# Optimization experiments

Measured on AMD Instinct MI355X. Metric: run time of the kernel, lower is better.

## Reference

```python
import jax, jax.numpy as jnp
import numpy as np

B, M, K, KNN = 2, 256, 64, 16
CXYZ, CFEAT = 3, 61
CIN = CXYZ + CFEAT  # 64
MLPS = [64, 128]
SUMM = sum(MLPS)    # 192
CALIB = 64
EXP = [256, 512]
OUT = 256
EPS = 1e-5


def bn(x, g, b):
    # BatchNorm eval mode with running_mean=0, running_var=1 (channel axis 1)
    shape = (1, -1) + (1,) * (x.ndim - 2)
    return x * (g / jnp.sqrt(1.0 + EPS)).reshape(shape) + b.reshape(shape)


def knn(x, k):
    xx = jnp.sum(x * x, axis=1)                      # (B, N)
    inner = jnp.einsum('bcn,bcm->bnm', x, x)         # (B, N, N)
    pd = 2.0 * inner - xx[:, :, None] - xx[:, None, :]
    return jax.lax.top_k(pd, k)[1]                   # (B, N, k)


def graph_feature(x, idx):
    # x: (B, C, N), idx: (B, N, k) -> (B, 2C, N, k)
    xt = jnp.transpose(x, (0, 2, 1))                 # (B, N, C)
    nb = jax.vmap(lambda a, i: a[i])(xt, idx)        # (B, N, k, C)
    ctr = xt[:, :, None, :]
    feat = jnp.concatenate([nb - ctr, jnp.broadcast_to(ctr, nb.shape)], axis=-1)
    return jnp.transpose(feat, (0, 3, 1, 2))


def forward(xyz, feats, e1_w, e1_g, e1_b, e2_w, e2_g, e2_b,
            cal1_w, cal1_g, cal1_b, cal2_w, cal2_bias,
            exp1_w, exp1_g, exp1_b, exp2_w, exp2_g, exp2_b,
            red_w, red_g, red_b, sc1_w, sc1_b, sc2_w, sc2_b,
            sc_n1_g, sc_n1_b, sc_n2_g, sc_n2_b):
    x3 = xyz.reshape(B * M, K, CXYZ).transpose(0, 2, 1)      # (BM, 3, K)
    f = feats.reshape(B * M, K, CFEAT).transpose(0, 2, 1)    # (BM, 61, K)
    idx = knn(x3, KNN)                                        # USE_FEATS_DIS=False: knn once on xyz
    x = jnp.concatenate([x3, f], axis=1)                      # (BM, 64, K)
    outs = []
    for W, g, b in ((e1_w, e1_g, e1_b), (e2_w, e2_g, e2_b)):
        gf = graph_feature(x, idx)                            # (BM, 2C, K, knn)
        y = jax.nn.relu(bn(jnp.einsum('oc,bcnk->bonk', W, gf), g, b))
        x = y.max(axis=-1)                                    # (BM, mlp_i, K)
        outs.append(x)
    x = jnp.concatenate(outs, axis=1)                         # (BM, 192, K)
    c = jax.nn.relu(bn(jnp.einsum('oc,bcn->bon', cal1_w, x), cal1_g, cal1_b))
    c = jnp.einsum('oc,bcn->bon', cal2_w, c) + cal2_bias[None, :, None]
    x = jax.nn.sigmoid(c) * x
    x = jax.nn.relu(bn(jnp.einsum('oc,bcn->bon', exp1_w, x), exp1_g, exp1_b))
    x = jax.nn.relu(bn(jnp.einsum('oc,bcn->bon', exp2_w, x), exp2_g, exp2_b))
    x = x.max(axis=-1).reshape(B, M, EXP[1]).transpose(0, 2, 1)  # (B, 512, M)
    x = jax.nn.relu(bn(jnp.einsum('oc,bcm->bom', red_w, x), red_g, red_b))
    x = bn(x + x, sc_n1_g, sc_n1_b)
    h = jax.nn.relu(jnp.einsum('oc,bcm->bom', sc1_w, x) + sc1_b[None, :, None])
    h = jnp.einsum('oc,bcm->bom', sc2_w, h) + sc2_b[None, :, None]
    x = bn(x + h, sc_n2_g, sc_n2_b)
    return x                                                  # (B, 256, M)


def setup_inputs() -> dict:
    key = jax.random.key(0)
    ks = jax.random.split(key, 16)
    w = lambda k, s: jax.random.normal(k, s, jnp.float32) * 0.05
    ones = lambda n: jnp.ones((n,), jnp.float32)
    zeros = lambda n: jnp.zeros((n,), jnp.float32)
    return {
        'xyz': jax.random.normal(ks[0], (B, M, K, CXYZ), jnp.float32),
        'feats': jax.random.normal(ks[1], (B, M, K, CFEAT), jnp.float32),
        'e1_w': w(ks[2], (MLPS[0], 2 * CIN)), 'e1_g': ones(MLPS[0]), 'e1_b': zeros(MLPS[0]),
        'e2_w': w(ks[3], (MLPS[1], 2 * MLPS[0])), 'e2_g': ones(MLPS[1]), 'e2_b': zeros(MLPS[1]),
        'cal1_w': w(ks[4], (CALIB, SUMM)), 'cal1_g': ones(CALIB), 'cal1_b': zeros(CALIB),
        'cal2_w': w(ks[5], (SUMM, CALIB)), 'cal2_bias': zeros(SUMM),
        'exp1_w': w(ks[6], (EXP[0], SUMM)), 'exp1_g': ones(EXP[0]), 'exp1_b': zeros(EXP[0]),
        'exp2_w': w(ks[7], (EXP[1], EXP[0])), 'exp2_g': ones(EXP[1]), 'exp2_b': zeros(EXP[1]),
        'red_w': w(ks[8], (OUT, EXP[1])), 'red_g': ones(OUT), 'red_b': zeros(OUT),
        'sc1_w': w(ks[9], (OUT, OUT)), 'sc1_b': zeros(OUT),
        'sc2_w': w(ks[10], (OUT, OUT)), 'sc2_b': zeros(OUT),
        'sc_n1_g': ones(OUT), 'sc_n1_b': zeros(OUT),
        'sc_n2_g': ones(OUT), 'sc_n2_b': zeros(OUT),
    }


def reference(xyz, feats, e1_w, e1_g, e1_b, e2_w, e2_g, e2_b,
              cal1_w, cal1_g, cal1_b, cal2_w, cal2_bias,
              exp1_w, exp1_g, exp1_b, exp2_w, exp2_g, exp2_b,
              red_w, red_g, red_b, sc1_w, sc1_b, sc2_w, sc2_b,
              sc_n1_g, sc_n1_b, sc_n2_g, sc_n2_b):
    return forward(xyz, feats, e1_w, e1_g, e1_b, e2_w, e2_g, e2_b,
                   cal1_w, cal1_g, cal1_b, cal2_w, cal2_bias,
                   exp1_w, exp1_g, exp1_b, exp2_w, exp2_g, exp2_b,
                   red_w, red_g, red_b, sc1_w, sc1_b, sc2_w, sc2_b,
                   sc_n1_g, sc_n1_b, sc_n2_g, sc_n2_b)
```

## Files before the change

kernel.cpp:

```cpp
#include <hip/hip_runtime.h>
#include <hip/hip_bf16.h>
#include <math.h>
#include <stddef.h>

#define DEV __device__ __forceinline__
__device__ const float BNS = 0.99999500003749968f;

typedef __bf16 bf16x8 __attribute__((ext_vector_type(8)));
typedef float  f32x4  __attribute__((ext_vector_type(4)));

DEV unsigned short f2bs(float v){
  union{ __hip_bfloat16 b; unsigned short u; } c; c.b=__float2bfloat16(v); return c.u;
}
DEV float bs2f(unsigned short u){
  union{ unsigned short u; __hip_bfloat16 b; } c; c.u=u; return __bfloat162float(c.b);
}


__global__ __launch_bounds__(256) void k_prep(const float* __restrict__ e1_w,
    const float* __restrict__ e2_w, const float* __restrict__ cal1_w,
    const float* __restrict__ cal2_w, const float* __restrict__ exp1_w,
    const float* __restrict__ exp2_w, unsigned short* __restrict__ Whi,
    unsigned short* __restrict__ Wlo){
  int bid = blockIdx.x;
  const float* src; unsigned short *hi,*lo; int mode, O=0, i0;
  if(bid<32)      { src=e1_w;  hi=Whi;       lo=Wlo;       mode=1; O= 64; i0=bid*256; }
  else if(bid<96) { src=e2_w;  hi=Whi+8192;  lo=Wlo+8192;  mode=1; O=128; i0=(bid-32)*256; }
  else if(bid<144){ src=cal1_w;hi=Whi+24576; lo=Wlo+24576; mode=0;        i0=(bid-96)*256; }
  else if(bid<192){ src=cal2_w;hi=Whi+36864; lo=Wlo+36864; mode=0;        i0=(bid-144)*256; }
  else if(bid<384){ src=exp1_w;hi=Whi+49152; lo=Wlo+49152; mode=0;        i0=(bid-192)*256; }
  else            { src=exp2_w;hi=Whi+98304; lo=Wlo+98304; mode=0;        i0=(bid-384)*256; }
  int i = i0 + threadIdx.x;
  float v;
  if(mode==0) v = src[i];
  else {
    int row=i>>6, c=i&63;
    v = (row<O) ? src[row*128+c] : (src[(row-O)*128+64+c]-src[(row-O)*128+c]);
  }
  unsigned short h=f2bs(v); hi[i]=h; lo[i]=f2bs(v-bs2f(h));
}

__global__ __launch_bounds__(256) void k_knn(const float* __restrict__ xyz,
    const float* __restrict__ feats, int* __restrict__ idxo,
    unsigned short* __restrict__ x0s){
  int bm = blockIdx.x;
  int tid = threadIdx.x, n = tid&63, s = tid>>6;
  __shared__ float sx0[64], sx1[64], sx2[64], sxx[64];
  __shared__ float pd[64][65];
  __shared__ float cv[64][4];
  __shared__ int   ci[64][4];
  __shared__ unsigned short sb[64*130];
  if(s==0){
    const float* xp = xyz + (size_t)(bm*64+n)*3;
    float px=xp[0], py=xp[1], pz=xp[2];
    sx0[n]=px; sx1[n]=py; sx2[n]=pz; sxx[n]=px*px+py*py+pz*pz;
  }
  __syncthreads();
  float px=sx0[n], py=sx1[n], pz=sx2[n], xxn=sxx[n];
  #pragma unroll
  for(int t=0;t<16;t++){
    int m = s*16+t;
    float inner = px*sx0[m]+py*sx1[m]+pz*sx2[m];
    pd[n][m] = 2.0f*inner - xxn - sxx[m];
  }
  __syncthreads();
  int* ip = idxo + bm*1024 + n*16;
  for(int j=0;j<16;j++){
    float best=-3.4e38f; int bi=s*16;
    #pragma unroll
    for(int t=0;t<16;t++){ int m=s*16+t; float v=pd[n][m]; if(v>best){best=v;bi=m;} }
    cv[n][s]=best; ci[n][s]=bi;
    __syncthreads();
    if(s==0){
      float bb=cv[n][0]; int bj=ci[n][0];
      #pragma unroll
      for(int q2=1;q2<4;q2++){ if(cv[n][q2]>bb){bb=cv[n][q2]; bj=ci[n][q2];} }
      ip[j]=bj; pd[n][bj]=-3.4e38f;
    }
    __syncthreads();
  }
  unsigned short* r = sb + n*130;
  if(s==0){
    unsigned short h;
    h=f2bs(px); r[0]=h; r[64]=f2bs(px-bs2f(h));
    h=f2bs(py); r[1]=h; r[65]=f2bs(py-bs2f(h));
    h=f2bs(pz); r[2]=h; r[66]=f2bs(pz-bs2f(h));
  }
  const float* fp = feats + (size_t)(bm*64+n)*61;
  #pragma unroll
  for(int t=0;t<16;t++){
    int cc = s*16+t;
    if(cc<61){
      float v=fp[cc]; unsigned short h=f2bs(v);
      r[3+cc]=h; r[64+3+cc]=f2bs(v-bs2f(h));
    }
  }
  __syncthreads();
  unsigned int* g32 = (unsigned int*)(x0s + (size_t)bm*8192);
  const unsigned int* s32 = (const unsigned int*)sb;
  #pragma unroll
  for(int t=0;t<16;t++){ int i=s*16+t; g32[i*64+n]=s32[i*65+n]; }
}

template<int O>
__global__ __launch_bounds__(256) void k_edge2(
    const unsigned short* __restrict__ Wh, const unsigned short* __restrict__ Wl,
    const unsigned short* __restrict__ X, int RS, int LO,
    const int* __restrict__ idxg, const float* __restrict__ gg,
    const float* __restrict__ bb, unsigned short* __restrict__ cat, int coloff){
  __shared__ float zs[64*65];
  __shared__ float ds[64*65];
  int bm = blockIdx.x;
  int tid = threadIdx.x, wid = tid>>6, lane = tid&63;
  int l15 = lane&15, q = lane>>4;
  const int* ip0 = idxg + bm*1024;
  size_t xrow = ((size_t)bm*64 + l15)*RS;
  for(int ch=0; ch<O/64; ch++){
    int rbase = ((wid<2)?0:O) + ch*64 + (wid&1)*32;
    f32x4 acc[2][4];
    #pragma unroll
    for(int a=0;a<2;a++)
      #pragma unroll
      for(int d=0;d<4;d++) acc[a][d]=(f32x4){0.f,0.f,0.f,0.f};
    #pragma unroll
    for(int kc=0;kc<2;kc++){
      int k0=kc*32;
      size_t a0=(size_t)(rbase+l15)*64 + k0 + q*8;
      size_t a1=(size_t)(rbase+16+l15)*64 + k0 + q*8;
      bf16x8 a0h=*(const bf16x8*)(Wh+a0), a0l=*(const bf16x8*)(Wl+a0);
      bf16x8 a1h=*(const bf16x8*)(Wh+a1), a1l=*(const bf16x8*)(Wl+a1);
      #pragma unroll
      for(int nt=0;nt<4;nt++){
        const unsigned short* xp = X + xrow + (size_t)nt*16*RS + k0 + q*8;
        bf16x8 bh=*(const bf16x8*)xp, bl=*(const bf16x8*)(xp+LO);
        acc[0][nt]=__builtin_amdgcn_mfma_f32_16x16x32_bf16(a0h,bh,acc[0][nt],0,0,0);
        acc[0][nt]=__builtin_amdgcn_mfma_f32_16x16x32_bf16(a0h,bl,acc[0][nt],0,0,0);
        acc[0][nt]=__builtin_amdgcn_mfma_f32_16x16x32_bf16(a0l,bh,acc[0][nt],0,0,0);
        acc[1][nt]=__builtin_amdgcn_mfma_f32_16x16x32_bf16(a1h,bh,acc[1][nt],0,0,0);
        acc[1][nt]=__builtin_amdgcn_mfma_f32_16x16x32_bf16(a1h,bl,acc[1][nt],0,0,0);
        acc[1][nt]=__builtin_amdgcn_mfma_f32_16x16x32_bf16(a1l,bh,acc[1][nt],0,0,0);
      }
    }
    __syncthreads();
    float* dst = (wid<2)? zs : ds;
    int ro = (wid&1)*32;
    #pragma unroll
    for(int mt=0;mt<2;mt++)
      #pragma unroll
      for(int nt=0;nt<4;nt++)
        #pragma unroll
        for(int rr=0;rr<4;rr++)
          dst[(ro+mt*16+q*4+rr)*65 + nt*16+l15] = acc[mt][nt][rr];
    __syncthreads();
    int o = ch*64 + lane;
    float s = gg[o]*BNS, bi = bb[o];
    #pragma unroll 4
    for(int j=0;j<16;j++){
      int n = wid*16 + j;
      const int* ip = ip0 + n*16;
      float mz = -3.4e38f;
      #pragma unroll
      for(int k=0;k<16;k++) mz = fmaxf(mz, zs[lane*65 + ip[k]]);
      float v = fmaxf(s*(mz + ds[lane*65 + n]) + bi, 0.f);
      unsigned short hv = f2bs(v);
      size_t cb = ((size_t)bm*64+n)*384 + coloff + o;
      cat[cb] = hv; cat[cb+192] = f2bs(v - bs2f(hv));
    }
    __syncthreads();
  }
}

template<int K, int BO, int EPI>
__global__ __launch_bounds__(256) void k_mm2(
    const unsigned short* __restrict__ Whi, const unsigned short* __restrict__ Wlo,
    const unsigned short* __restrict__ X, void* __restrict__ Og,
    const float* __restrict__ sg, const float* __restrict__ bg, int O){
  constexpr int WO = BO/4;
  constexpr int MT = WO/16;
  constexpr int WUNITS = BO*8;
  __shared__ __align__(16) unsigned short sW[BO*64];
  __shared__ __align__(16) unsigned short sX[128*64];
  int rt = blockIdx.x;
  int o0 = blockIdx.y*BO;
  int tid = threadIdx.x, wid = tid>>6, lane = tid&63;
  int l15 = lane&15, q = lane>>4;
  f32x4 acc[MT][8];
  #pragma unroll
  for(int a=0;a<MT;a++)
    #pragma unroll
    for(int d=0;d<8;d++) acc[a][d]=(f32x4){0.f,0.f,0.f,0.f};
  size_t xbase = (size_t)rt*128*2*K;
  for(int kc=0; kc<K/32; kc++){
    int k0 = kc*32;
    __syncthreads();
    #pragma unroll
    for(int i=0;i<WUNITS/256;i++){
      int U = tid + i*256;
      int r = U>>3, up = U&7, u = up ^ (r&7);
      const unsigned short* src = (u<4)
        ? (Whi + (size_t)(o0+r)*K + k0 + u*8)
        : (Wlo + (size_t)(o0+r)*K + k0 + (u-4)*8);
      *(uint4*)&sW[U*8] = *(const uint4*)src;
    }
    #pragma unroll
    for(int i=0;i<4;i++){
      int U = tid + i*256;
      int r = U>>3, up = U&7, u = up ^ (r&7);
      const unsigned short* src = X + xbase + (size_t)r*2*K
        + (u<4 ? (size_t)(k0 + u*8) : (size_t)(K + k0 + (u-4)*8));
      *(uint4*)&sX[U*8] = *(const uint4*)src;
    }
    __syncthreads();
    bf16x8 wf[MT][2];
    #pragma unroll
    for(int mt=0;mt<MT;mt++){
      int o = wid*WO + mt*16 + l15;
      wf[mt][0] = *(const bf16x8*)&sW[(o*8 + ((  q) ^ (o&7)))*8];
      wf[mt][1] = *(const bf16x8*)&sW[(o*8 + ((4+q) ^ (o&7)))*8];
    }
    #pragma unroll
    for(int nf=0;nf<8;nf++){
      int r = nf*16 + l15;
      bf16x8 xh = *(const bf16x8*)&sX[(r*8 + ((  q) ^ (r&7)))*8];
      bf16x8 xl = *(const bf16x8*)&sX[(r*8 + ((4+q) ^ (r&7)))*8];
      #pragma unroll
      for(int mt=0;mt<MT;mt++){
        acc[mt][nf]=__builtin_amdgcn_mfma_f32_16x16x32_bf16(wf[mt][0],xh,acc[mt][nf],0,0,0);
        acc[mt][nf]=__builtin_amdgcn_mfma_f32_16x16x32_bf16(wf[mt][0],xl,acc[mt][nf],0,0,0);
        acc[mt][nf]=__builtin_amdgcn_mfma_f32_16x16x32_bf16(wf[mt][1],xh,acc[mt][nf],0,0,0);
      }
    }
  }
  if(EPI==0){
    unsigned short* ob = (unsigned short*)Og;
    #pragma unroll
    for(int mt=0;mt<MT;mt++){
      int ob0 = o0 + wid*WO + mt*16 + q*4;
      float s0[4], b0[4];
      #pragma unroll
      for(int r=0;r<4;r++){ s0[r]=sg[ob0+r]*BNS; b0[r]=bg[ob0+r]; }
      #pragma unroll
      for(int nf=0;nf<8;nf++){
        size_t row = (size_t)rt*128 + nf*16 + l15;
        size_t rb = row*2*O;
        unsigned short hv[4], lv[4];
        #pragma unroll
        for(int r=0;r<4;r++){
          float v = fmaxf(acc[mt][nf][r]*s0[r]+b0[r], 0.f);
          hv[r]=f2bs(v); lv[r]=f2bs(v - bs2f(hv[r]));
        }
        *(ushort4*)(ob + rb + ob0)     = make_ushort4(hv[0],hv[1],hv[2],hv[3]);
        *(ushort4*)(ob + rb + O + ob0) = make_ushort4(lv[0],lv[1],lv[2],lv[3]);
      }
    }
  } else if(EPI==1){
    unsigned short* cat = (unsigned short*)Og;
    #pragma unroll
    for(int mt=0;mt<MT;mt++){
      int ob0 = o0 + wid*WO + mt*16 + q*4;
      float bi[4];
      #pragma unroll
      for(int r=0;r<4;r++) bi[r]=sg[ob0+r];
      #pragma unroll
      for(int nf=0;nf<8;nf++){
        size_t row = (size_t)rt*128 + nf*16 + l15;
        size_t rb = row*384;
        ushort4 hv = *(ushort4*)(cat + rb + ob0);
        ushort4 lv = *(ushort4*)(cat + rb + 192 + ob0);
        unsigned short h[4]={hv.x,hv.y,hv.z,hv.w}, l[4]={lv.x,lv.y,lv.z,lv.w};
        #pragma unroll
        for(int r=0;r<4;r++){
          float g = 1.f/(1.f+__expf(-(acc[mt][nf][r]+bi[r])));
          float f = (bs2f(h[r])+bs2f(l[r]))*g;
          h[r]=f2bs(f); l[r]=f2bs(f-bs2f(h[r]));
        }
        *(ushort4*)(cat + rb + ob0)       = make_ushort4(h[0],h[1],h[2],h[3]);
        *(ushort4*)(cat + rb + 192 + ob0) = make_ushort4(l[0],l[1],l[2],l[3]);
      }
    }
  } else {
    float* pool = (float*)Og;
    #pragma unroll
    for(int mt=0;mt<MT;mt++){
      int ob0 = o0 + wid*WO + mt*16 + q*4;
      #pragma unroll
      for(int half=0;half<2;half++){
        int bm = 2*rt + half;
        int b = bm>>8, m = bm&255;
        #pragma unroll
        for(int r=0;r<4;r++){
          float s=sg[ob0+r]*BNS, bi=bg[ob0+r];
          float v = acc[mt][half*4+0][r]*s+bi;
          v = fmaxf(v, acc[mt][half*4+1][r]*s+bi);
          v = fmaxf(v, acc[mt][half*4+2][r]*s+bi);
          v = fmaxf(v, acc[mt][half*4+3][r]*s+bi);
          v = fmaxf(v, 0.f);
          v = fmaxf(v, __shfl_xor(v,1));
          v = fmaxf(v, __shfl_xor(v,2));
          v = fmaxf(v, __shfl_xor(v,4));
          v = fmaxf(v, __shfl_xor(v,8));
          if(l15==0) pool[((size_t)b*512 + ob0+r)*256 + m] = v;
        }
      }
    }
  }
}

__global__ __launch_bounds__(256) void k_tr3(const float* __restrict__ red_w,
    const float* __restrict__ sc1_w, const float* __restrict__ sc2_w,
    float* __restrict__ Wt_red, float* __restrict__ Wt_s1, float* __restrict__ Wt_s2){
  __shared__ float s[32][33];
  int bid=blockIdx.x;
  const float* in; float* out; int O,K,lb;
  if(bid<128){ in=red_w; out=Wt_red; O=256; K=512; lb=bid; }
  else if(bid<192){ in=sc1_w; out=Wt_s1; O=256; K=256; lb=bid-128; }
  else { in=sc2_w; out=Wt_s2; O=256; K=256; lb=bid-192; }
  int nt=O>>5;
  int to=lb%nt, tk=lb/nt;
  int c=threadIdx.x&31, r8=threadIdx.x>>5;
  #pragma unroll
  for(int p=0;p<4;p++){
    int r=r8+p*8;
    s[r][c]=in[(size_t)(to*32+r)*K + tk*32 + c];
  }
  __syncthreads();
  #pragma unroll
  for(int p=0;p<4;p++){
    int r=r8+p*8;
    out[(size_t)(tk*32+r)*O + to*32 + c]=s[c][r];
  }
}

template<int EPI>
__global__ __launch_bounds__(256) void k_head(const float* __restrict__ Wt,
    const float* __restrict__ Xg, float* __restrict__ Og,
    const float* __restrict__ p0, const float* __restrict__ p1,
    const float* __restrict__ p2, const float* __restrict__ p3,
    const float* __restrict__ res, int O, int K){
  __shared__ float As[32][64];
  __shared__ float Bs[32][32];
  int not_ = O>>6;
  int g = blockIdx.x / not_, ot = blockIdx.x % not_;
  int b = g>>3, mg = g&7;
  int o0 = ot*64;
  int tid=threadIdx.x, tx=tid&7, ty=tid>>3;
  float acc[2][4];
  #pragma unroll
  for(int a=0;a<2;a++)
    #pragma unroll
    for(int d=0;d<4;d++) acc[a][d]=0.f;
  const float* Xb = Xg + (size_t)b*K*256 + mg*32;
  for(int k0=0;k0<K;k0+=32){
    __syncthreads();
    #pragma unroll
    for(int p=0;p<2;p++){
      int r = p*16 + (tid>>4), c4 = (tid&15)*4;
      *(float4*)&As[r][c4] = *(const float4*)&Wt[(size_t)(k0+r)*O + o0 + c4];
    }
    {
      int r = tid>>3, c4 = (tid&7)*4;
      *(float4*)&Bs[r][c4] = *(const float4*)&Xb[(size_t)(k0+r)*256 + c4];
    }
    __syncthreads();
    #pragma unroll
    for(int k=0;k<32;k++){
      float av[2], bv[4];
      av[0]=As[k][ty*2]; av[1]=As[k][ty*2+1];
      #pragma unroll
      for(int d=0;d<4;d++) bv[d]=Bs[k][tx*4+d];
      #pragma unroll
      for(int a=0;a<2;a++)
        #pragma unroll
        for(int d=0;d<4;d++) acc[a][d]+=av[a]*bv[d];
    }
  }
  int m0 = mg*32 + tx*4;
  #pragma unroll
  for(int a=0;a<2;a++){
    int o=o0+ty*2+a;
    float* orow = Og + ((size_t)b*O + o)*256 + m0;
    float v[4];
    if(EPI==0){
      float s=p0[o]*BNS, bi=p1[o], s1=p2[o]*BNS, b1=p3[o];
      #pragma unroll
      for(int d=0;d<4;d++){ float r=fmaxf(acc[a][d]*s+bi,0.f); v[d]=2.f*r*s1+b1; }
    } else if(EPI==1){
      float bi=p0[o];
      #pragma unroll
      for(int d=0;d<4;d++) v[d]=fmaxf(acc[a][d]+bi,0.f);
    } else {
      float bi=p0[o], s2=p1[o]*BNS, b2=p2[o];
      const float* rr = res + ((size_t)b*O + o)*256 + m0;
      #pragma unroll
      for(int d=0;d<4;d++){ float u=rr[d]+acc[a][d]+bi; v[d]=u*s2+b2; }
    }
    *(float4*)orow = make_float4(v[0],v[1],v[2],v[3]);
  }
}

extern "C" void kernel_launch(void* const* d_in, const int* in_sizes, int n_in,
                              void* d_out, int out_size, void* d_ws, size_t ws_size,
                              hipStream_t stream){
  const float* xyz     =(const float*)d_in[0];
  const float* feats   =(const float*)d_in[1];
  const float* e1_w    =(const float*)d_in[2];
  const float* e1_g    =(const float*)d_in[3];
  const float* e1_b    =(const float*)d_in[4];
  const float* e2_w    =(const float*)d_in[5];
  const float* e2_g    =(const float*)d_in[6];
  const float* e2_b    =(const float*)d_in[7];
  const float* cal1_w  =(const float*)d_in[8];
  const float* cal1_g  =(const float*)d_in[9];
  const float* cal1_b  =(const float*)d_in[10];
  const float* cal2_w  =(const float*)d_in[11];
  const float* cal2_bias=(const float*)d_in[12];
  const float* exp1_w  =(const float*)d_in[13];
  const float* exp1_g  =(const float*)d_in[14];
  const float* exp1_b  =(const float*)d_in[15];
  const float* exp2_w  =(const float*)d_in[16];
  const float* exp2_g  =(const float*)d_in[17];
  const float* exp2_b  =(const float*)d_in[18];
  const float* red_w   =(const float*)d_in[19];
  const float* red_g   =(const float*)d_in[20];
  const float* red_b   =(const float*)d_in[21];
  const float* sc1_w   =(const float*)d_in[22];
  const float* sc1_b   =(const float*)d_in[23];
  const float* sc2_w   =(const float*)d_in[24];
  const float* sc2_b   =(const float*)d_in[25];
  const float* sc_n1_g =(const float*)d_in[26];
  const float* sc_n1_b =(const float*)d_in[27];
  const float* sc_n2_g =(const float*)d_in[28];
  const float* sc_n2_b =(const float*)d_in[29];

  char* wsb=(char*)d_ws;
  int*            idx =(int*)           (wsb);
  unsigned short* x0s =(unsigned short*)(wsb + 2097152);
  unsigned short* c1s = x0s;
  unsigned short* cats=(unsigned short*)(wsb + 10485760);
  unsigned short* p1s =(unsigned short*)(wsb + 35651584);
  float*          pool=(float*)         (wsb + 69206016);
  float*          x1  =(float*)         (wsb + 70254592);
  float*          hbuf=(float*)         (wsb + 70778880);
  unsigned short* Whi =(unsigned short*)(wsb + 70254592);
  unsigned short* Wlo =(unsigned short*)(wsb + 70713344);
  float*          Wt_red=(float*)       (wsb);
  float*          Wt_s1 =(float*)       (wsb + 524288);
  float*          Wt_s2 =(float*)       (wsb + 786432);
  unsigned short* e1e_h=Whi;          unsigned short* e1e_l=Wlo;
  unsigned short* e2e_h=Whi+8192;     unsigned short* e2e_l=Wlo+8192;
  unsigned short* c1w_h=Whi+24576;    unsigned short* c1w_l=Wlo+24576;
  unsigned short* c2w_h=Whi+36864;    unsigned short* c2w_l=Wlo+36864;
  unsigned short* e1w_h=Whi+49152;    unsigned short* e1w_l=Wlo+49152;
  unsigned short* e2w_h=Whi+98304;    unsigned short* e2w_l=Wlo+98304;

  k_prep      <<<896,256,0,stream>>>(e1_w,e2_w,cal1_w,cal2_w,exp1_w,exp2_w,Whi,Wlo);
  k_knn       <<<512,256,0,stream>>>(xyz,feats,idx,x0s);
  k_edge2< 64><<<512,256,0,stream>>>(e1e_h,e1e_l,x0s, 128, 64,idx,e1_g,e1_b,cats, 0);
  k_edge2<128><<<512,256,0,stream>>>(e2e_h,e2e_l,cats,384,192,idx,e2_g,e2_b,cats,64);
  k_tr3       <<<256,256,0,stream>>>(red_w,sc1_w,sc2_w,Wt_red,Wt_s1,Wt_s2);
  k_mm2<192, 64,0><<<dim3(256,1),256,0,stream>>>(c1w_h,c1w_l,cats,(void*)c1s,cal1_g,cal1_b, 64);
  k_mm2< 64, 64,1><<<dim3(256,3),256,0,stream>>>(c2w_h,c2w_l,c1s,(void*)cats,cal2_bias,cal2_bias,192);
  k_mm2<192,128,0><<<dim3(256,2),256,0,stream>>>(e1w_h,e1w_l,cats,(void*)p1s,exp1_g,exp1_b,256);
  k_mm2<256,128,2><<<dim3(256,4),256,0,stream>>>(e2w_h,e2w_l,p1s,(void*)pool,exp2_g,exp2_b,512);
  k_head<0>   <<< 64,256,0,stream>>>(Wt_red,pool,x1,  red_g,red_b,sc_n1_g,sc_n1_b,nullptr,256,512);
  k_head<1>   <<< 64,256,0,stream>>>(Wt_s1, x1,  hbuf,sc1_b,nullptr,nullptr,nullptr,nullptr,256,256);
  k_head<2>   <<< 64,256,0,stream>>>(Wt_s2, hbuf,(float*)d_out,sc2_b,sc_n2_g,sc_n2_b,nullptr,x1,256,256);
}
```

Baseline: 295.8 us.

## Fuse calibration GEMMs into one kernel and merge weight transpose into prep

Replaces the two calibration GEMM launches (cal1 then cal2 with sigmoid gating) with a single kernel that keeps the 64-channel intermediate in shared memory, so it no longer makes a global round trip. The weight-transpose kernel is folded into the weight-prep launch as extra blocks, and the workspace layout is moved to avoid overlap. The exp2 GEMM switches to a 256-wide output tile with half the grid in y. These changes cut launches and global traffic, but the larger tile raises register pressure and the fused kernel uses more LDS, which may reduce occupancy.

```diff
diff --git a/kernel.cpp b/kernel.cpp
--- a/kernel.cpp
+++ b/kernel.cpp
@@ -21,23 +21,49 @@
     const float* __restrict__ e2_w, const float* __restrict__ cal1_w,
     const float* __restrict__ cal2_w, const float* __restrict__ exp1_w,
     const float* __restrict__ exp2_w, unsigned short* __restrict__ Whi,
-    unsigned short* __restrict__ Wlo){
+    unsigned short* __restrict__ Wlo,
+    const float* __restrict__ red_w, const float* __restrict__ sc1_w,
+    const float* __restrict__ sc2_w, float* __restrict__ Wt_red,
+    float* __restrict__ Wt_s1, float* __restrict__ Wt_s2){
+  __shared__ float s[32][33];
   int bid = blockIdx.x;
-  const float* src; unsigned short *hi,*lo; int mode, O=0, i0;
-  if(bid<32)      { src=e1_w;  hi=Whi;       lo=Wlo;       mode=1; O= 64; i0=bid*256; }
-  else if(bid<96) { src=e2_w;  hi=Whi+8192;  lo=Wlo+8192;  mode=1; O=128; i0=(bid-32)*256; }
-  else if(bid<144){ src=cal1_w;hi=Whi+24576; lo=Wlo+24576; mode=0;        i0=(bid-96)*256; }
-  else if(bid<192){ src=cal2_w;hi=Whi+36864; lo=Wlo+36864; mode=0;        i0=(bid-144)*256; }
-  else if(bid<384){ src=exp1_w;hi=Whi+49152; lo=Wlo+49152; mode=0;        i0=(bid-192)*256; }
-  else            { src=exp2_w;hi=Whi+98304; lo=Wlo+98304; mode=0;        i0=(bid-384)*256; }
-  int i = i0 + threadIdx.x;
-  float v;
-  if(mode==0) v = src[i];
-  else {
-    int row=i>>6, c=i&63;
-    v = (row<O) ? src[row*128+c] : (src[(row-O)*128+64+c]-src[(row-O)*128+c]);
-  }
-  unsigned short h=f2bs(v); hi[i]=h; lo[i]=f2bs(v-bs2f(h));
+  if(bid < 896){
+    const float* src; unsigned short *hi,*lo; int mode, O=0, i0;
+    if(bid<32)      { src=e1_w;  hi=Whi;       lo=Wlo;       mode=1; O= 64; i0=bid*256; }
+    else if(bid<96) { src=e2_w;  hi=Whi+8192;  lo=Wlo+8192;  mode=1; O=128; i0=(bid-32)*256; }
+    else if(bid<144){ src=cal1_w;hi=Whi+24576; lo=Wlo+24576; mode=0;        i0=(bid-96)*256; }
+    else if(bid<192){ src=cal2_w;hi=Whi+36864; lo=Wlo+36864; mode=0;        i0=(bid-144)*256; }
+    else if(bid<384){ src=exp1_w;hi=Whi+49152; lo=Wlo+49152; mode=0;        i0=(bid-192)*256; }
+    else            { src=exp2_w;hi=Whi+98304; lo=Wlo+98304; mode=0;        i0=(bid-384)*256; }
+    int i = i0 + threadIdx.x;
+    float v;
+    if(mode==0) v = src[i];
+    else {
+      int row=i>>6, c=i&63;
+      v = (row<O) ? src[row*128+c] : (src[(row-O)*128+64+c]-src[(row-O)*128+c]);
+    }
+    unsigned short h=f2bs(v); Whi=hi; Wlo=lo; hi[i]=h; lo[i]=f2bs(v-bs2f(h));
+  } else {
+    int lb = bid-896;
+    const float* in; float* out; int O,K;
+    if(lb<128){ in=red_w; out=Wt_red; O=256; K=512; }
+    else if(lb<192){ in=sc1_w; out=Wt_s1; O=256; K=256; lb-=128; }
+    else { in=sc2_w; out=Wt_s2; O=256; K=256; lb-=192; }
+    int nt=O>>5;
+    int to=lb%nt, tk=lb/nt;
+    int c=threadIdx.x&31, r8=threadIdx.x>>5;
+    #pragma unroll
+    for(int p=0;p<4;p++){
+      int r=r8+p*8;
+      s[r][c]=in[(size_t)(to*32+r)*K + tk*32 + c];
+    }
+    __syncthreads();
+    #pragma unroll
+    for(int p=0;p<4;p++){
+      int r=r8+p*8;
+      out[(size_t)(tk*32+r)*O + to*32 + c]=s[c][r];
+    }
+  }
 }
 
 __global__ __launch_bounds__(256) void k_knn(const float* __restrict__ xyz,
@@ -170,6 +196,129 @@
   }
 }
 
+__global__ __launch_bounds__(256) void k_cal(
+    const unsigned short* __restrict__ Whi, const unsigned short* __restrict__ Wlo,
+    unsigned short* __restrict__ cats,
+    const float* __restrict__ c1g, const float* __restrict__ c1b,
+    const float* __restrict__ c2bias){
+  const unsigned short* c1w_h = Whi+24576; const unsigned short* c1w_l = Wlo+24576;
+  const unsigned short* c2w_h = Whi+36864; const unsigned short* c2w_l = Wlo+36864;
+  __shared__ __align__(16) unsigned short sW[64*64];
+  __shared__ __align__(16) unsigned short sX[128*64];
+  __shared__ __align__(16) unsigned short c1L[128*136];
+  int rt = blockIdx.x;
+  int tid = threadIdx.x, wid = tid>>6, lane = tid&63;
+  int l15 = lane&15, q = lane>>4;
+  f32x4 acc1[8];
+  #pragma unroll
+  for(int d=0;d<8;d++) acc1[d]=(f32x4){0.f,0.f,0.f,0.f};
+  size_t xbase = (size_t)rt*128*384;
+  for(int kc=0;kc<6;kc++){
+    int k0=kc*32;
+    __syncthreads();
+    #pragma unroll
+    for(int i=0;i<2;i++){
+      int U = tid + i*256;
+      int r = U>>3, up = U&7, u = up ^ (r&7);
+      const unsigned short* src = (u<4)
+        ? (c1w_h + (size_t)r*192 + k0 + u*8)
+        : (c1w_l + (size_t)r*192 + k0 + (u-4)*8);
+      *(uint4*)&sW[U*8] = *(const uint4*)src;
+    }
+    #pragma unroll
+    for(int i=0;i<4;i++){
+      int U = tid + i*256;
+      int r = U>>3, up = U&7, u = up ^ (r&7);
+      const unsigned short* src = cats + xbase + (size_t)r*384
+        + (u<4 ? (size_t)(k0 + u*8) : (size_t)(192 + k0 + (u-4)*8));
+      *(uint4*)&sX[U*8] = *(const uint4*)src;
+    }
+    __syncthreads();
+    int o = wid*16 + l15;
+    bf16x8 wh = *(const bf16x8*)&sW[(o*8 + ((  q) ^ (o&7)))*8];
+    bf16x8 wl = *(const bf16x8*)&sW[(o*8 + ((4+q) ^ (o&7)))*8];
+    #pragma unroll
+    for(int nf=0;nf<8;nf++){
+      int r = nf*16 + l15;
+      bf16x8 xh = *(const bf16x8*)&sX[(r*8 + ((  q) ^ (r&7)))*8];
+      bf16x8 xl = *(const bf16x8*)&sX[(r*8 + ((4+q) ^ (r&7)))*8];
+      acc1[nf]=__builtin_amdgcn_mfma_f32_16x16x32_bf16(wh,xh,acc1[nf],0,0,0);
+      acc1[nf]=__builtin_amdgcn_mfma_f32_16x16x32_bf16(wh,xl,acc1[nf],0,0,0);
+      acc1[nf]=__builtin_amdgcn_mfma_f32_16x16x32_bf16(wl,xh,acc1[nf],0,0,0);
+    }
+  }
+  {
+    int ob0 = wid*16 + q*4;
+    float s0[4], b0[4];
+    #pragma unroll
+    for(int r=0;r<4;r++){ s0[r]=c1g[ob0+r]*BNS; b0[r]=c1b[ob0+r]; }
+    #pragma unroll
+    for(int nf=0;nf<8;nf++){
+      int n = nf*16 + l15;
+      unsigned short hv[4], lv[4];
+      #pragma unroll
+      for(int r=0;r<4;r++){
+        float v = fmaxf(acc1[nf][r]*s0[r]+b0[r], 0.f);
+        hv[r]=f2bs(v); lv[r]=f2bs(v - bs2f(hv[r]));
+      }
+      *(ushort4*)&c1L[n*136 + ob0]      = make_ushort4(hv[0],hv[1],hv[2],hv[3]);
+      *(ushort4*)&c1L[n*136 + 64 + ob0] = make_ushort4(lv[0],lv[1],lv[2],lv[3]);
+    }
+  }
+  __syncthreads();
+  f32x4 acc2[3][8];
+  #pragma unroll
+  for(int a=0;a<3;a++)
+    #pragma unroll
+    for(int d=0;d<8;d++) acc2[a][d]=(f32x4){0.f,0.f,0.f,0.f};
+  #pragma unroll
+  for(int kc=0;kc<2;kc++){
+    int k0=kc*32;
+    bf16x8 ah[3], al[3];
+    #pragma unroll
+    for(int mt=0;mt<3;mt++){
+      int o = wid*48 + mt*16 + l15;
+      ah[mt]=*(const bf16x8*)(c2w_h + (size_t)o*64 + k0 + q*8);
+      al[mt]=*(const bf16x8*)(c2w_l + (size_t)o*64 + k0 + q*8);
+    }
+    #pragma unroll
+    for(int nf=0;nf<8;nf++){
+      int n = nf*16 + l15;
+      bf16x8 bh = *(const bf16x8*)&c1L[n*136 + k0 + q*8];
+      bf16x8 bl = *(const bf16x8*)&c1L[n*136 + 64 + k0 + q*8];
+      #pragma unroll
+      for(int mt=0;mt<3;mt++){
+        acc2[mt][nf]=__builtin_amdgcn_mfma_f32_16x16x32_bf16(ah[mt],bh,acc2[mt][nf],0,0,0);
+        acc2[mt][nf]=__builtin_amdgcn_mfma_f32_16x16x32_bf16(ah[mt],bl,acc2[mt][nf],0,0,0);
+        acc2[mt][nf]=__builtin_amdgcn_mfma_f32_16x16x32_bf16(al[mt],bh,acc2[mt][nf],0,0,0);
+      }
+    }
+  }
+  #pragma unroll
+  for(int mt=0;mt<3;mt++){
+    int ob0 = wid*48 + mt*16 + q*4;
+    float bi[4];
+    #pragma unroll
+    for(int r=0;r<4;r++) bi[r]=c2bias[ob0+r];
+    #pragma unroll
+    for(int nf=0;nf<8;nf++){
+      size_t row = (size_t)rt*128 + nf*16 + l15;
+      size_t rb = row*384;
+      ushort4 hv = *(ushort4*)(cats + rb + ob0);
+      ushort4 lv = *(ushort4*)(cats + rb + 192 + ob0);
+      unsigned short h[4]={hv.x,hv.y,hv.z,hv.w}, l[4]={lv.x,lv.y,lv.z,lv.w};
+      #pragma unroll
+      for(int r=0;r<4;r++){
+        float g = 1.f/(1.f+__expf(-(acc2[mt][nf][r]+bi[r])));
+        float f = (bs2f(h[r])+bs2f(l[r]))*g;
+        h[r]=f2bs(f); l[r]=f2bs(f-bs2f(h[r]));
+      }
+      *(ushort4*)(cats + rb + ob0)       = make_ushort4(h[0],h[1],h[2],h[3]);
+      *(ushort4*)(cats + rb + 192 + ob0) = make_ushort4(l[0],l[1],l[2],l[3]);
+    }
+  }
+}
+
 template<int K, int BO, int EPI>
 __global__ __launch_bounds__(256) void k_mm2(
     const unsigned short* __restrict__ Whi, const unsigned short* __restrict__ Wlo,
@@ -251,31 +400,6 @@
         }
         *(ushort4*)(ob + rb + ob0)     = make_ushort4(hv[0],hv[1],hv[2],hv[3]);
         *(ushort4*)(ob + rb + O + ob0) = make_ushort4(lv[0],lv[1],lv[2],lv[3]);
-      }
-    }
-  } else if(EPI==1){
-    unsigned short* cat = (unsigned short*)Og;
-    #pragma unroll
-    for(int mt=0;mt<MT;mt++){
-      int ob0 = o0 + wid*WO + mt*16 + q*4;
-      float bi[4];
-      #pragma unroll
-      for(int r=0;r<4;r++) bi[r]=sg[ob0+r];
-      #pragma unroll
-      for(int nf=0;nf<8;nf++){
-        size_t row = (size_t)rt*128 + nf*16 + l15;
-        size_t rb = row*384;
-        ushort4 hv = *(ushort4*)(cat + rb + ob0);
-        ushort4 lv = *(ushort4*)(cat + rb + 192 + ob0);
-        unsigned short h[4]={hv.x,hv.y,hv.z,hv.w}, l[4]={lv.x,lv.y,lv.z,lv.w};
-        #pragma unroll
-        for(int r=0;r<4;r++){
-          float g = 1.f/(1.f+__expf(-(acc[mt][nf][r]+bi[r])));
-          float f = (bs2f(h[r])+bs2f(l[r]))*g;
-          h[r]=f2bs(f); l[r]=f2bs(f-bs2f(h[r]));
-        }
-        *(ushort4*)(cat + rb + ob0)       = make_ushort4(h[0],h[1],h[2],h[3]);
-        *(ushort4*)(cat + rb + 192 + ob0) = make_ushort4(l[0],l[1],l[2],l[3]);
       }
     }
   } else {
@@ -303,31 +427,6 @@
         }
       }
     }
-  }
-}
-
-__global__ __launch_bounds__(256) void k_tr3(const float* __restrict__ red_w,
-    const float* __restrict__ sc1_w, const float* __restrict__ sc2_w,
-    float* __restrict__ Wt_red, float* __restrict__ Wt_s1, float* __restrict__ Wt_s2){
-  __shared__ float s[32][33];
-  int bid=blockIdx.x;
-  const float* in; float* out; int O,K,lb;
-  if(bid<128){ in=red_w; out=Wt_red; O=256; K=512; lb=bid; }
-  else if(bid<192){ in=sc1_w; out=Wt_s1; O=256; K=256; lb=bid-128; }
-  else { in=sc2_w; out=Wt_s2; O=256; K=256; lb=bid-192; }
-  int nt=O>>5;
-  int to=lb%nt, tk=lb/nt;
-  int c=threadIdx.x&31, r8=threadIdx.x>>5;
-  #pragma unroll
-  for(int p=0;p<4;p++){
-    int r=r8+p*8;
-    s[r][c]=in[(size_t)(to*32+r)*K + tk*32 + c];
-  }
-  __syncthreads();
-  #pragma unroll
-  for(int p=0;p<4;p++){
-    int r=r8+p*8;
-    out[(size_t)(tk*32+r)*O + to*32 + c]=s[c][r];
   }
 }
 
@@ -435,33 +534,29 @@
   char* wsb=(char*)d_ws;
   int*            idx =(int*)           (wsb);
   unsigned short* x0s =(unsigned short*)(wsb + 2097152);
-  unsigned short* c1s = x0s;
   unsigned short* cats=(unsigned short*)(wsb + 10485760);
   unsigned short* p1s =(unsigned short*)(wsb + 35651584);
   float*          pool=(float*)         (wsb + 69206016);
   float*          x1  =(float*)         (wsb + 70254592);
   float*          hbuf=(float*)         (wsb + 70778880);
-  unsigned short* Whi =(unsigned short*)(wsb + 70254592);
-  unsigned short* Wlo =(unsigned short*)(wsb + 70713344);
-  float*          Wt_red=(float*)       (wsb);
-  float*          Wt_s1 =(float*)       (wsb + 524288);
-  float*          Wt_s2 =(float*)       (wsb + 786432);
+  unsigned short* Whi =(unsigned short*)(wsb + 75497472);
+  unsigned short* Wlo =(unsigned short*)(wsb + 76021760);
+  float*          Wt_red=(float*)       (wsb + 76546048);
+  float*          Wt_s1 =(float*)       (wsb + 77070336);
+  float*          Wt_s2 =(float*)       (wsb + 77332480);
   unsigned short* e1e_h=Whi;          unsigned short* e1e_l=Wlo;
   unsigned short* e2e_h=Whi+8192;     unsigned short* e2e_l=Wlo+8192;
-  unsigned short* c1w_h=Whi+24576;    unsigned short* c1w_l=Wlo+24576;
-  unsigned short* c2w_h=Whi+36864;    unsigned short* c2w_l=Wlo+36864;
   unsigned short* e1w_h=Whi+49152;    unsigned short* e1w_l=Wlo+49152;
   unsigned short* e2w_h=Whi+98304;    unsigned short* e2w_l=Wlo+98304;
 
-  k_prep      <<<896,256,0,stream>>>(e1_w,e2_w,cal1_w,cal2_w,exp1_w,exp2_w,Whi,Wlo);
+  k_prep      <<<1152,256,0,stream>>>(e1_w,e2_w,cal1_w,cal2_w,exp1_w,exp2_w,Whi,Wlo,
+                                      red_w,sc1_w,sc2_w,Wt_red,Wt_s1,Wt_s2);
   k_knn       <<<512,256,0,stream>>>(xyz,feats,idx,x0s);
   k_edge2< 64><<<512,256,0,stream>>>(e1e_h,e1e_l,x0s, 128, 64,idx,e1_g,e1_b,cats, 0);
   k_edge2<128><<<512,256,0,stream>>>(e2e_h,e2e_l,cats,384,192,idx,e2_g,e2_b,cats,64);
-  k_tr3       <<<256,256,0,stream>>>(red_w,sc1_w,sc2_w,Wt_red,Wt_s1,Wt_s2);
-  k_mm2<192, 64,0><<<dim3(256,1),256,0,stream>>>(c1w_h,c1w_l,cats,(void*)c1s,cal1_g,cal1_b, 64);
-  k_mm2< 64, 64,1><<<dim3(256,3),256,0,stream>>>(c2w_h,c2w_l,c1s,(void*)cats,cal2_bias,cal2_bias,192);
+  k_cal       <<<256,256,0,stream>>>(Whi,Wlo,cats,cal1_g,cal1_b,cal2_bias);
   k_mm2<192,128,0><<<dim3(256,2),256,0,stream>>>(e1w_h,e1w_l,cats,(void*)p1s,exp1_g,exp1_b,256);
-  k_mm2<256,128,2><<<dim3(256,4),256,0,stream>>>(e2w_h,e2w_l,p1s,(void*)pool,exp2_g,exp2_b,512);
+  k_mm2<256,256,2><<<dim3(256,2),256,0,stream>>>(e2w_h,e2w_l,p1s,(void*)pool,exp2_g,exp2_b,512);
   k_head<0>   <<< 64,256,0,stream>>>(Wt_red,pool,x1,  red_g,red_b,sc_n1_g,sc_n1_b,nullptr,256,512);
   k_head<1>   <<< 64,256,0,stream>>>(Wt_s1, x1,  hbuf,sc1_b,nullptr,nullptr,nullptr,nullptr,256,256);
   k_head<2>   <<< 64,256,0,stream>>>(Wt_s2, hbuf,(float*)d_out,sc2_b,sc_n2_g,sc_n2_b,nullptr,x1,256,256);
```

New measurement: 303.2 us. 2.5% more time.
